# Optimization experiments

Measured on AMD Instinct MI355X. Metric: run time of the kernel, lower is better.

Reference implementation:

```python
import jax, jax.numpy as jnp
import numpy as np

N_NODES = 100000
N_INCID = 2000000
N_HEDGES = 300000
IN_DIM = 92
H_DIM = 64
ATTR_DIM = 35
HOUT_DIM = 128
N_GRAPHS = 512
N_LAYERS = 3
MSG_DIM = 2 * H_DIM + ATTR_DIM  # 163, matches Linear(2*node_fea_dim+hedge_fea_dim, out_dim)


def _segment_mean(vals, ids, num_segments):
    s = jax.ops.segment_sum(vals, ids, num_segments=num_segments)
    c = jax.ops.segment_sum(jnp.ones((vals.shape[0],), vals.dtype), ids, num_segments=num_segments)
    return s / jnp.maximum(c, 1.0)[:, None]


def setup_inputs() -> dict:
    key = jax.random.key(0)
    ks = jax.random.split(key, 16)
    x = jax.random.normal(ks[0], (N_NODES, IN_DIM), jnp.float32)
    incid_nodes = jax.random.randint(ks[1], (N_INCID,), 0, N_NODES)
    incid_hedges = jax.random.randint(ks[2], (N_INCID,), 0, N_HEDGES)
    hedge_attr = jax.random.normal(ks[3], (N_HEDGES, ATTR_DIM), jnp.float32)
    batch = jnp.sort(jax.random.randint(ks[4], (N_NODES,), 0, N_GRAPHS))
    def lin(k, fi, fo):
        lim = 1.0 / np.sqrt(fi)
        kw, kb = jax.random.split(k)
        return (jax.random.uniform(kw, (fi, fo), jnp.float32, -lim, lim),
                jax.random.uniform(kb, (fo,), jnp.float32, -lim, lim))
    W_embed, b_embed = lin(ks[5], IN_DIM, H_DIM)
    Wf, bf = [], []
    Wc, bc = [], []
    for l in range(N_LAYERS):
        w, b = lin(jax.random.fold_in(ks[6], l), MSG_DIM, H_DIM)
        Wf.append(w); bf.append(b)
        w, b = lin(jax.random.fold_in(ks[7], l), MSG_DIM, H_DIM)
        Wc.append(w); bc.append(b)
    Wf = jnp.stack(Wf); bf = jnp.stack(bf)
    Wc = jnp.stack(Wc); bc = jnp.stack(bc)
    W_proj, b_proj = lin(ks[8], H_DIM, HOUT_DIM)
    W_out, b_out = lin(ks[9], HOUT_DIM, 1)
    return {"x": x, "incid_nodes": incid_nodes, "incid_hedges": incid_hedges,
            "hedge_attr": hedge_attr, "batch": batch,
            "W_embed": W_embed, "b_embed": b_embed,
            "Wf": Wf, "bf": bf, "Wc": Wc, "bc": bc,
            "W_proj": W_proj, "b_proj": b_proj, "W_out": W_out, "b_out": b_out}


def reference(x, incid_nodes, incid_hedges, hedge_attr, batch,
              W_embed, b_embed, Wf, bf, Wc, bc, W_proj, b_proj, W_out, b_out):
    h = x @ W_embed + b_embed  # [N, H_DIM] embed
    node_cnt = jax.ops.segment_sum(jnp.ones((N_INCID,), h.dtype), incid_nodes,
                                   num_segments=N_NODES)
    has_incid = (node_cnt > 0)[:, None]
    # mean of hedge_attr over hedges containing each node (constant across layers)
    node_a = _segment_mean(hedge_attr[incid_hedges], incid_nodes, N_NODES)
    for l in range(N_LAYERS):
        # per-hedge mean of member node features (the normalized node_hedge_adj @ x)
        hedge_mean = _segment_mean(h[incid_nodes], incid_hedges, N_HEDGES)  # [H, H_DIM]
        # per-node mean over incident hedges of the message components
        node_h = _segment_mean(hedge_mean[incid_hedges], incid_nodes, N_NODES)
        x_part = jnp.where(has_incid, h, 0.0)  # mean over incidences of constant x_i
        z = jnp.concatenate([x_part, node_h, node_a], axis=1)  # [N, MSG_DIM]
        z_f = z @ Wf[l] + bf[l]
        z_c = z @ Wc[l] + bc[l]
        h = jax.nn.softplus(jax.nn.sigmoid(z_f) * jax.nn.softplus(z_c) + h)
    pooled = _segment_mean(h, batch, N_GRAPHS)  # scatter-mean global pooling
    p = jax.nn.softplus(pooled @ W_proj + b_proj)
    return p @ W_out + b_out  # [N_GRAPHS, 1]
```

## Files before the change

kernel.cpp:

```cpp
#include <hip/hip_runtime.h>
#include <hip/hip_bf16.h>

#define N_NODES 100000
#define N_INCID 2000000
#define N_HEDGES 300000
#define IN_DIM 92
#define H_DIM 64
#define ATTR_DIM 35
#define ATTR_PAIRS 18
#define HOUT_DIM 128
#define N_GRAPHS 512
#define N_LAYERS 3
#define MSG_DIM 163
#define KPAIRS 96
#define ZLDS 100
#define EPAIRS 48
#define ELDS 50

#define IPB 8192
#define NBLK 245
#define ESHIFT 9
#define NB_E 586
#define NSHIFT 8
#define NB_N 391
#define VALBITS 21

typedef short bf16x8 __attribute__((ext_vector_type(8)));
typedef float f32x4 __attribute__((ext_vector_type(4)));

__device__ __forceinline__ float softplusf(float x) {
    return fmaxf(x, 0.f) + __logf(1.f + __expf(-fabsf(x)));
}
__device__ __forceinline__ float sigmoidf(float x) {
    return __builtin_amdgcn_rcpf(1.f + __expf(-x));
}
__device__ __forceinline__ float u2f(unsigned u) {
    union { unsigned u; float f; } x; x.u = u; return x.f;
}
__device__ __forceinline__ unsigned f2_to_bf2(float x, float y) {
    union { float f; unsigned u; } a, b;
    a.f = x; b.f = y;
    unsigned lo = (a.u + 0x7fffu + ((a.u >> 16) & 1u)) >> 16;
    unsigned hi = ((b.u + 0x7fffu + ((b.u >> 16) & 1u)) >> 16) << 16;
    return lo | hi;
}

__global__ void embpack_k(const float* __restrict__ W, unsigned* __restrict__ BtE) {
    int idx = blockIdx.x * 256 + threadIdx.x;
    if (idx >= 64 * EPAIRS) return;
    int c = idx / EPAIRS, p = idx - c * EPAIRS;
    int k0 = 2 * p, k1 = 2 * p + 1;
    float v0 = (k0 < IN_DIM) ? W[k0 * 64 + c] : 0.f;
    float v1 = (k1 < IN_DIM) ? W[k1 * 64 + c] : 0.f;
    BtE[idx] = f2_to_bf2(v0, v1);
}

__global__ void __launch_bounds__(256)
embed_mfma_k(const float* __restrict__ x, const unsigned* __restrict__ BtE,
             const float* __restrict__ be, const int* __restrict__ ncnt,
             float* __restrict__ h, unsigned* __restrict__ hb,
             unsigned* __restrict__ zb) {
    __shared__ unsigned zsu[64][ELDS];
    __shared__ unsigned btu[64][ELDS];
    int node0 = blockIdx.x * 64;
    int t = threadIdx.x;
    for (int idx = t; idx < 64 * EPAIRS; idx += 256) {
        int r = idx / EPAIRS, p = idx - r * EPAIRS;
        int node = node0 + r;
        unsigned pr = 0u;
        if (node < N_NODES && p < 46) {
            float2 f = *(const float2*)(x + (size_t)node * IN_DIM + 2 * p);
            pr = f2_to_bf2(f.x, f.y);
        }
        zsu[r][p] = pr;
    }
    for (int idx = t; idx < 64 * EPAIRS; idx += 256) {
        int c = idx / EPAIRS, p = idx - c * EPAIRS;
        btu[c][p] = BtE[idx];
    }
    __syncthreads();
    int w = t >> 6, lane = t & 63, row16 = lane & 15, kg = lane >> 4;
    f32x4 acc[4];
#pragma unroll
    for (int n = 0; n < 4; ++n) acc[n] = (f32x4){0.f, 0.f, 0.f, 0.f};
#pragma unroll
    for (int ks = 0; ks < 3; ++ks) {
        int pbase = ks * 16 + kg * 4;
        bf16x8 a = *(const bf16x8*)&zsu[w * 16 + row16][pbase];
#pragma unroll
        for (int n = 0; n < 4; ++n) {
            bf16x8 b = *(const bf16x8*)&btu[n * 16 + row16][pbase];
            acc[n] = __builtin_amdgcn_mfma_f32_16x16x32_bf16(a, b, acc[n], 0, 0, 0);
        }
    }
#pragma unroll
    for (int i = 0; i < 4; ++i) {
        int node = node0 + w * 16 + kg * 4 + i;
        if (node < N_NODES) {
            bool has = ncnt[node] > 0;
#pragma unroll
            for (int n = 0; n < 4; ++n) {
                int d = n * 16 + row16;
                float nv = acc[n][i] + be[d];
                h[node * 64 + d] = nv;
                float other = __shfl_xor(nv, 1);
                if ((d & 1) == 0) {
                    unsigned pr = f2_to_bf2(nv, other);
                    hb[node * 32 + (d >> 1)] = pr;
                    zb[(size_t)node * KPAIRS + (d >> 1)] = has ? pr : 0u;
                }
            }
        }
    }
}

__global__ void attrconv_k(const float* __restrict__ hattr, unsigned* __restrict__ hab) {
    int idx = blockIdx.x * 256 + threadIdx.x;
    if (idx >= N_HEDGES * ATTR_PAIRS) return;
    int e = idx / ATTR_PAIRS, p = idx - e * ATTR_PAIRS;
    int d0 = 2 * p, d1 = 2 * p + 1;
    float v0 = hattr[e * ATTR_DIM + d0];
    float v1 = (d1 < ATTR_DIM) ? hattr[e * ATTR_DIM + d1] : 0.f;
    hab[idx] = f2_to_bf2(v0, v1);
}

__global__ void btpack_k(const float* __restrict__ Wf, const float* __restrict__ Wc,
                         unsigned* __restrict__ Btb) {
    int idx = blockIdx.x * 256 + threadIdx.x;
    if (idx >= N_LAYERS * 128 * KPAIRS) return;
    int l = idx / (128 * KPAIRS);
    int rem = idx - l * 128 * KPAIRS;
    int c = rem / KPAIRS, p = rem - c * KPAIRS;
    int k0 = 2 * p, k1 = 2 * p + 1;
    const float* W = (c < 64) ? (Wf + (size_t)l * MSG_DIM * 64) : (Wc + (size_t)l * MSG_DIM * 64);
    int cc = c & 63;
    float v0 = (k0 < MSG_DIM) ? W[k0 * 64 + cc] : 0.f;
    float v1 = (k1 < MSG_DIM) ? W[k1 * 64 + cc] : 0.f;
    Btb[idx] = f2_to_bf2(v0, v1);
}

__global__ void sorthist_k(const int* __restrict__ key, int* __restrict__ hist,
                           int kshift, int NB) {
    __shared__ int cnt[640];
    int blk = blockIdx.x;
    for (int i = threadIdx.x; i < NB; i += 256) cnt[i] = 0;
    __syncthreads();
    int base = blk * IPB;
    int end = min(base + IPB, N_INCID);
    for (int i = base + threadIdx.x; i < end; i += 256)
        atomicAdd(&cnt[key[i] >> kshift], 1);
    __syncthreads();
    for (int i = threadIdx.x; i < NB; i += 256) hist[blk * NB + i] = cnt[i];
}

__global__ void scanR1_k(const int* __restrict__ in, int* __restrict__ out,
                         int* __restrict__ bsum, int n, int NB) {
    __shared__ int tmp[256];
    int gid = blockIdx.x * 256 + threadIdx.x;
    int v = 0;
    if (gid < n) {
        int bucket = gid / NBLK, blk = gid - bucket * NBLK;
        v = in[blk * NB + bucket];
    }
    tmp[threadIdx.x] = v;
    __syncthreads();
    for (int o = 1; o < 256; o <<= 1) {
        int t = (threadIdx.x >= o) ? tmp[threadIdx.x - o] : 0;
        __syncthreads();
        tmp[threadIdx.x] += t;
        __syncthreads();
    }
    if (gid < n) out[gid] = tmp[threadIdx.x] - v;
    if (threadIdx.x == 255) bsum[blockIdx.x] = tmp[255];
}

__global__ void scan2_k(int* __restrict__ bsum, int nb) {
    __shared__ int tmp[256];
    __shared__ int carry;
    if (threadIdx.x == 0) carry = 0;
    __syncthreads();
    for (int base = 0; base < nb; base += 256) {
        int gid = base + threadIdx.x;
        int v = (gid < nb) ? bsum[gid] : 0;
        tmp[threadIdx.x] = v;
        __syncthreads();
        for (int o = 1; o < 256; o <<= 1) {
            int t = (threadIdx.x >= o) ? tmp[threadIdx.x - o] : 0;
            __syncthreads();
            tmp[threadIdx.x] += t;
            __syncthreads();
        }
        if (gid < nb) bsum[gid] = tmp[threadIdx.x] - v + carry;
        __syncthreads();
        if (threadIdx.x == 0) carry += tmp[255];
        __syncthreads();
    }
}

__global__ void scan3_k(int* __restrict__ out, const int* __restrict__ bsum, int n) {
    int gid = blockIdx.x * 256 + threadIdx.x;
    if (gid < n) out[gid] += bsum[blockIdx.x];
}

__global__ void sortscat_k(const int* __restrict__ key, const int* __restrict__ val,
                           const int* __restrict__ soff, unsigned* __restrict__ stage,
                           int kshift, int NB) {
    __shared__ int cur[640], bas[640];
    int blk = blockIdx.x;
    for (int i = threadIdx.x; i < NB; i += 256) {
        cur[i] = 0;
        bas[i] = soff[i * NBLK + blk];
    }
    __syncthreads();
    int base = blk * IPB;
    int end = min(base + IPB, N_INCID);
    unsigned kmaskbits = (1u << kshift) - 1u;
    for (int i = base + threadIdx.x; i < end; i += 256) {
        int k = key[i], b = k >> kshift;
        int d = bas[b] + atomicAdd(&cur[b], 1);
        stage[d] = (((unsigned)k & kmaskbits) << VALBITS) | (unsigned)val[i];
    }
}

__global__ void sortfine_k(const unsigned* __restrict__ stage, const int* __restrict__ soff,
                           int* __restrict__ csr, int* __restrict__ koff,
                           float* __restrict__ krcp, int* __restrict__ kcnt,
                           int kshift, int NB, int NKEYS) {
    __shared__ int cnt[512], off[512], cur[512];
    __shared__ int ts[256];
    int b = blockIdx.x;
    int tid = threadIdx.x;
    int KPB = 1 << kshift;
    int kbase = b << kshift;
    int base = soff[b * NBLK];
    int end = (b == NB - 1) ? N_INCID : soff[(b + 1) * NBLK];
    for (int i = tid; i < KPB; i += 256) cnt[i] = 0;
    __syncthreads();
    for (int i = base + tid; i < end; i += 256)
        atomicAdd(&cnt[stage[i] >> VALBITS], 1);
    __syncthreads();
    int half = KPB >> 1;
    int c0 = 0, c1 = 0;
    if (tid < half) { c0 = cnt[2 * tid]; c1 = cnt[2 * tid + 1]; ts[tid] = c0 + c1; }
    __syncthreads();
    for (int o = 1; o < 256; o <<= 1) {
        int v = (tid >= o && tid < half) ? ts[tid - o] : 0;
        __syncthreads();
        if (tid < half) ts[tid] += v;
        __syncthreads();
    }
    if (tid < half) {
        int ex = ts[tid] - (c0 + c1);
        off[2 * tid] = ex;
        off[2 * tid + 1] = ex + c0;
    }
    __syncthreads();
    for (int k = tid; k < KPB; k += 256) {
        int gk = kbase + k;
        if (gk < NKEYS) {
            koff[gk] = base + off[k];
            krcp[gk] = 1.0f / (float)max(cnt[k], 1);
            kcnt[gk] = cnt[k];
        }
        cur[k] = 0;
    }
    __syncthreads();
    for (int i = base + tid; i < end; i += 256) {
        unsigned it = stage[i];
        int lk = (int)(it >> VALBITS);
        int pos = base + off[lk] + atomicAdd(&cur[lk], 1);
        csr[pos] = (int)(it & ((1u << VALBITS) - 1u));
    }
}

__global__ void sentinel_k(int* __restrict__ eoff, int* __restrict__ noff) {
    if (threadIdx.x == 0) eoff[N_HEDGES] = N_INCID;
    if (threadIdx.x == 1) noff[N_NODES] = N_INCID;
}

__global__ void hmean_k(const int* __restrict__ eoff, const int* __restrict__ csr_en,
                        const uint4* __restrict__ hbv4, const float* __restrict__ ercp,
                        uint4* __restrict__ hmv4) {
    int idx = blockIdx.x * 256 + threadIdx.x;
    int e = idx >> 5, l = idx & 31;
    if (e >= N_HEDGES) return;
    int sub = l >> 3, q = l & 7;
    int s = eoff[e], t = eoff[e + 1];
    float a0 = 0, a1 = 0, a2 = 0, a3 = 0, a4 = 0, a5 = 0, a6 = 0, a7 = 0;
    for (int base = s; base < t; base += 32) {
        int cnt = min(32, t - base);
        int myidx = (base + l < t) ? csr_en[base + l] : 0;
        for (int j = 0; j < cnt; j += 16) {
            uint4 v[4];
#pragma unroll
            for (int w = 0; w < 4; ++w) {
                int mem = j + 4 * w + sub;
                int nq = __shfl(myidx, mem, 32);
                v[w] = (mem < cnt) ? hbv4[nq * 8 + q] : make_uint4(0u, 0u, 0u, 0u);
            }
#pragma unroll
            for (int w = 0; w < 4; ++w) {
                a0 += u2f(v[w].x << 16); a1 += u2f(v[w].x);
                a2 += u2f(v[w].y << 16); a3 += u2f(v[w].y);
                a4 += u2f(v[w].z << 16); a5 += u2f(v[w].z);
                a6 += u2f(v[w].w << 16); a7 += u2f(v[w].w);
            }
        }
    }
    a0 += __shfl_xor(a0, 8); a0 += __shfl_xor(a0, 16);
    a1 += __shfl_xor(a1, 8); a1 += __shfl_xor(a1, 16);
    a2 += __shfl_xor(a2, 8); a2 += __shfl_xor(a2, 16);
    a3 += __shfl_xor(a3, 8); a3 += __shfl_xor(a3, 16);
    a4 += __shfl_xor(a4, 8); a4 += __shfl_xor(a4, 16);
    a5 += __shfl_xor(a5, 8); a5 += __shfl_xor(a5, 16);
    a6 += __shfl_xor(a6, 8); a6 += __shfl_xor(a6, 16);
    a7 += __shfl_xor(a7, 8); a7 += __shfl_xor(a7, 16);
    if (sub == 0) {
        float rc = ercp[e];
        hmv4[e * 8 + q] = make_uint4(f2_to_bf2(a0 * rc, a1 * rc), f2_to_bf2(a2 * rc, a3 * rc),
                                     f2_to_bf2(a4 * rc, a5 * rc), f2_to_bf2(a6 * rc, a7 * rc));
    }
}

__global__ void nodeh_k(const int* __restrict__ noff, const int* __restrict__ csr_ne,
                        const uint4* __restrict__ hmv4, const float* __restrict__ nrcp,
                        uint4* __restrict__ zbv4) {
    int idx = blockIdx.x * 256 + threadIdx.x;
    int n = idx >> 5, l = idx & 31;
    if (n >= N_NODES) return;
    int sub = l >> 3, q = l & 7;
    int s = noff[n], t = noff[n + 1];
    float a0 = 0, a1 = 0, a2 = 0, a3 = 0, a4 = 0, a5 = 0, a6 = 0, a7 = 0;
    for (int base = s; base < t; base += 32) {
        int cnt = min(32, t - base);
        int myidx = (base + l < t) ? csr_ne[base + l] : 0;
        for (int j = 0; j < cnt; j += 16) {
            uint4 v[4];
#pragma unroll
            for (int w = 0; w < 4; ++w) {
                int mem = j + 4 * w + sub;
                int eq = __shfl(myidx, mem, 32);
                v[w] = (mem < cnt) ? hmv4[eq * 8 + q] : make_uint4(0u, 0u, 0u, 0u);
            }
#pragma unroll
            for (int w = 0; w < 4; ++w) {
                a0 += u2f(v[w].x << 16); a1 += u2f(v[w].x);
                a2 += u2f(v[w].y << 16); a3 += u2f(v[w].y);
                a4 += u2f(v[w].z << 16); a5 += u2f(v[w].z);
                a6 += u2f(v[w].w << 16); a7 += u2f(v[w].w);
            }
        }
    }
    a0 += __shfl_xor(a0, 8); a0 += __shfl_xor(a0, 16);
    a1 += __shfl_xor(a1, 8); a1 += __shfl_xor(a1, 16);
    a2 += __shfl_xor(a2, 8); a2 += __shfl_xor(a2, 16);
    a3 += __shfl_xor(a3, 8); a3 += __shfl_xor(a3, 16);
    a4 += __shfl_xor(a4, 8); a4 += __shfl_xor(a4, 16);
    a5 += __shfl_xor(a5, 8); a5 += __shfl_xor(a5, 16);
    a6 += __shfl_xor(a6, 8); a6 += __shfl_xor(a6, 16);
    a7 += __shfl_xor(a7, 8); a7 += __shfl_xor(a7, 16);
    if (sub == 0) {
        float rc = nrcp[n];
        zbv4[(size_t)n * 24 + 8 + q] =
            make_uint4(f2_to_bf2(a0 * rc, a1 * rc), f2_to_bf2(a2 * rc, a3 * rc),
                       f2_to_bf2(a4 * rc, a5 * rc), f2_to_bf2(a6 * rc, a7 * rc));
    }
}

__global__ void nodea_k(const int* __restrict__ noff, const int* __restrict__ csr_ne,
                        const uint2* __restrict__ habv, const float* __restrict__ nrcp,
                        uint2* __restrict__ zbv) {
    int idx = blockIdx.x * 256 + threadIdx.x;
    int n = idx >> 5, l = idx & 31;
    if (n >= N_NODES) return;
    int sub = l >> 4, q = l & 15;
    bool act = (q < ATTR_PAIRS / 2);
    int s = noff[n], t = noff[n + 1];
    float a0 = 0.f, a1 = 0.f, a2 = 0.f, a3 = 0.f;
    for (int base = s; base < t; base += 32) {
        int cnt = min(32, t - base);
        int myidx = (base + l < t) ? csr_ne[base + l] : 0;
        for (int j = 0; j < cnt; j += 16) {
            uint2 v[8];
#pragma unroll
            for (int w = 0; w < 8; ++w) {
                int mem = j + 2 * w + sub;
                int eq = __shfl(myidx, mem, 32);
                v[w] = (act && mem < cnt) ? habv[eq * (ATTR_PAIRS / 2) + q] : make_uint2(0u, 0u);
            }
#pragma unroll
            for (int w = 0; w < 8; ++w) {
                a0 += u2f(v[w].x << 16); a1 += u2f(v[w].x);
                a2 += u2f(v[w].y << 16); a3 += u2f(v[w].y);
            }
        }
    }
    a0 += __shfl_xor(a0, 16);
    a1 += __shfl_xor(a1, 16);
    a2 += __shfl_xor(a2, 16);
    a3 += __shfl_xor(a3, 16);
    if (sub == 0) {
        float rc = nrcp[n];
        uint2 pr = act ? make_uint2(f2_to_bf2(a0 * rc, a1 * rc), f2_to_bf2(a2 * rc, a3 * rc))
                       : make_uint2(0u, 0u);
        zbv[(size_t)n * (KPAIRS / 2) + 32 + q] = pr;
    }
}

__global__ void __launch_bounds__(256)
layer_mfma_k(const unsigned* __restrict__ Btl, const float* __restrict__ bfv,
             const float* __restrict__ bcv, const int* __restrict__ ncnt,
             unsigned* __restrict__ zb, float* __restrict__ h,
             unsigned* __restrict__ hb) {
    __shared__ unsigned zsu[64][ZLDS];
    int node0 = blockIdx.x * 64;
    int t = threadIdx.x;
    int w = t >> 6, lane = t & 63;
    int row16 = lane & 15, kg = lane >> 4;

    uint4 bregF[6], bregC[6];
    {
        const uint4* bv = (const uint4*)Btl;
        int colF = w * 16 + row16;
        int colC = colF + 64;
#pragma unroll
        for (int ks = 0; ks < 6; ++ks) {
            bregF[ks] = bv[colF * 24 + ks * 4 + kg];
            bregC[ks] = bv[colC * 24 + ks * 4 + kg];
        }
    }
    {
        const uint4* zv = (const uint4*)zb;
        for (int idx = t; idx < 64 * 24; idx += 256) {
            int r = idx / 24, p4 = idx - r * 24;
            int node = node0 + r;
            uint4 v = make_uint4(0u, 0u, 0u, 0u);
            if (node < N_NODES) v = zv[(size_t)node * 24 + p4];
            *(uint4*)&zsu[r][p4 * 4] = v;
        }
    }
    __syncthreads();

    f32x4 accF[4], accC[4];
#pragma unroll
    for (int n = 0; n < 4; ++n) {
        accF[n] = (f32x4){0.f, 0.f, 0.f, 0.f};
        accC[n] = (f32x4){0.f, 0.f, 0.f, 0.f};
    }

#pragma unroll
    for (int ks = 0; ks < 6; ++ks) {
        int pbase = ks * 16 + kg * 4;
        bf16x8 bF = *(const bf16x8*)&bregF[ks];
        bf16x8 bC = *(const bf16x8*)&bregC[ks];
#pragma unroll
        for (int rb = 0; rb < 4; ++rb) {
            bf16x8 a = *(const bf16x8*)&zsu[rb * 16 + row16][pbase];
            accF[rb] = __builtin_amdgcn_mfma_f32_16x16x32_bf16(a, bF, accF[rb], 0, 0, 0);
            accC[rb] = __builtin_amdgcn_mfma_f32_16x16x32_bf16(a, bC, accC[rb], 0, 0, 0);
        }
    }

    int d = w * 16 + row16;
    float bfd = bfv[d], bcd = bcv[d];
#pragma unroll
    for (int rb = 0; rb < 4; ++rb) {
#pragma unroll
        for (int i = 0; i < 4; ++i) {
            int node = node0 + rb * 16 + kg * 4 + i;
            if (node < N_NODES) {
                bool has = ncnt[node] > 0;
                float f = accF[rb][i] + bfd;
                float c = accC[rb][i] + bcd;
                float hv = h[node * 64 + d];
                float nv = softplusf(sigmoidf(f) * softplusf(c) + hv);
                h[node * 64 + d] = nv;
                float other = __shfl_xor(nv, 1);
                if ((d & 1) == 0) {
                    unsigned pr = f2_to_bf2(nv, other);
                    hb[node * 32 + (d >> 1)] = pr;
                    zb[(size_t)node * KPAIRS + (d >> 1)] = has ? pr : 0u;
                }
            }
        }
    }
}

__global__ void gstart_k(const int* __restrict__ batch, int* __restrict__ gstart) {
    int g = blockIdx.x * 256 + threadIdx.x;
    if (g > N_GRAPHS) return;
    int lo = 0, hi = N_NODES;
    while (lo < hi) {
        int mid = (lo + hi) >> 1;
        if (batch[mid] < g) lo = mid + 1; else hi = mid;
    }
    gstart[g] = lo;
}

__global__ void poolhead_k(const float* __restrict__ h, const int* __restrict__ gstart,
                           const float* __restrict__ Wp, const float* __restrict__ bp,
                           const float* __restrict__ Wo, const float* __restrict__ bo,
                           float* __restrict__ out) {
    __shared__ float partial[4][64];
    __shared__ float pm[64];
    __shared__ float pr[128];
    int g = blockIdx.x, t = threadIdx.x;
    int s = gstart[g], e = gstart[g + 1];
    int w = t >> 6, lane = t & 63;
    float acc = 0.f;
    for (int n = s + w; n < e; n += 4) acc += h[n * 64 + lane];
    partial[w][lane] = acc;
    __syncthreads();
    if (t < 64) {
        float c = fmaxf((float)(e - s), 1.0f);
        pm[t] = (partial[0][t] + partial[1][t] + partial[2][t] + partial[3][t]) / c;
    }
    __syncthreads();
    if (t < 128) {
        float a = bp[t];
#pragma unroll 4
        for (int k = 0; k < 64; ++k) a += pm[k] * Wp[k * HOUT_DIM + t];
        pr[t] = softplusf(a) * Wo[t];
    }
    __syncthreads();
    if (t < 64) {
        float v = pr[t] + pr[t + 64];
        for (int o = 32; o > 0; o >>= 1) v += __shfl_down(v, o);
        if (t == 0) out[g] = v + bo[0];
    }
}

extern "C" void kernel_launch(void* const* d_in, const int* in_sizes, int n_in,
                              void* d_out, int out_size, void* d_ws, size_t ws_size,
                              hipStream_t stream) {
    const float* x       = (const float*)d_in[0];
    const int*   inc_n   = (const int*)d_in[1];
    const int*   inc_e   = (const int*)d_in[2];
    const float* hattr   = (const float*)d_in[3];
    const int*   batch   = (const int*)d_in[4];
    const float* W_embed = (const float*)d_in[5];
    const float* b_embed = (const float*)d_in[6];
    const float* Wf      = (const float*)d_in[7];
    const float* bf      = (const float*)d_in[8];
    const float* Wc      = (const float*)d_in[9];
    const float* bc      = (const float*)d_in[10];
    const float* W_proj  = (const float*)d_in[11];
    const float* b_proj  = (const float*)d_in[12];
    const float* W_out   = (const float*)d_in[13];
    const float* b_out   = (const float*)d_in[14];
    float* out = (float*)d_out;

    char* ws = (char*)d_ws;
    size_t off = 0;
    auto alloc = [&](size_t bytes) {
        void* p = ws + off;
        off = (off + bytes + 255) & ~(size_t)255;
        return p;
    };
    float*    h      = (float*)alloc((size_t)N_NODES * 64 * 4);
    unsigned* hb     = (unsigned*)alloc((size_t)N_NODES * 32 * 4);
    unsigned* hmean  = (unsigned*)alloc((size_t)N_HEDGES * 32 * 4);
    unsigned* zb     = (unsigned*)alloc((size_t)N_NODES * KPAIRS * 4);
    unsigned* hab    = (unsigned*)alloc((size_t)N_HEDGES * ATTR_PAIRS * 4);
    unsigned* Btb    = (unsigned*)alloc((size_t)N_LAYERS * 128 * KPAIRS * 4);
    unsigned* BtE    = (unsigned*)alloc((size_t)64 * EPAIRS * 4);
    int*      ncnt   = (int*)alloc((size_t)N_NODES * 4);
    int*      ecnt   = (int*)alloc((size_t)N_HEDGES * 4);
    float*    nrcp   = (float*)alloc((size_t)N_NODES * 4);
    float*    ercp   = (float*)alloc((size_t)N_HEDGES * 4);
    int*      eoff   = (int*)alloc((size_t)(N_HEDGES + 1) * 4);
    int*      noff   = (int*)alloc((size_t)(N_NODES + 1) * 4);
    int*      csr_en = (int*)alloc((size_t)N_INCID * 4);
    int*      csr_ne = (int*)alloc((size_t)N_INCID * 4);
    int*      hist   = (int*)alloc((size_t)NB_E * NBLK * 4);
    int*      soff   = (int*)alloc((size_t)NB_E * NBLK * 4);
    int*      bsum   = (int*)alloc((size_t)2048 * 4);
    int*      gstart = (int*)alloc((size_t)(N_GRAPHS + 1) * 4);
    unsigned* stage  = (unsigned*)hmean;

    {
        int nlog = NB_E * NBLK;
        int nsb = (nlog + 255) / 256;
        sorthist_k<<<NBLK, 256, 0, stream>>>(inc_e, hist, ESHIFT, NB_E);
        scanR1_k<<<nsb, 256, 0, stream>>>(hist, soff, bsum, nlog, NB_E);
        scan2_k<<<1, 256, 0, stream>>>(bsum, nsb);
        scan3_k<<<nsb, 256, 0, stream>>>(soff, bsum, nlog);
        sortscat_k<<<NBLK, 256, 0, stream>>>(inc_e, inc_n, soff, stage, ESHIFT, NB_E);
        sortfine_k<<<NB_E, 256, 0, stream>>>(stage, soff, csr_en, eoff, ercp, ecnt,
                                             ESHIFT, NB_E, N_HEDGES);
    }
    {
        int nlog = NB_N * NBLK;
        int nsb = (nlog + 255) / 256;
        sorthist_k<<<NBLK, 256, 0, stream>>>(inc_n, hist, NSHIFT, NB_N);
        scanR1_k<<<nsb, 256, 0, stream>>>(hist, soff, bsum, nlog, NB_N);
        scan2_k<<<1, 256, 0, stream>>>(bsum, nsb);
        scan3_k<<<nsb, 256, 0, stream>>>(soff, bsum, nlog);
        sortscat_k<<<NBLK, 256, 0, stream>>>(inc_n, inc_e, soff, stage, NSHIFT, NB_N);
        sortfine_k<<<NB_N, 256, 0, stream>>>(stage, soff, csr_ne, noff, nrcp, ncnt,
                                             NSHIFT, NB_N, N_NODES);
    }
    sentinel_k<<<1, 64, 0, stream>>>(eoff, noff);

    embpack_k<<<(64 * EPAIRS + 255) / 256, 256, 0, stream>>>(W_embed, BtE);
    embed_mfma_k<<<(N_NODES + 63) / 64, 256, 0, stream>>>(x, BtE, b_embed, ncnt, h, hb, zb);
    attrconv_k<<<(N_HEDGES * ATTR_PAIRS + 255) / 256, 256, 0, stream>>>(hattr, hab);
    btpack_k<<<(N_LAYERS * 128 * KPAIRS + 255) / 256, 256, 0, stream>>>(Wf, Wc, Btb);
    nodea_k<<<(N_NODES * 32) / 256, 256, 0, stream>>>(noff, csr_ne, (const uint2*)hab, nrcp,
                                                      (uint2*)zb);

    for (int l = 0; l < N_LAYERS; ++l) {
        hmean_k<<<(N_HEDGES * 32) / 256, 256, 0, stream>>>(eoff, csr_en, (const uint4*)hb, ercp,
                                                           (uint4*)hmean);
        nodeh_k<<<(N_NODES * 32) / 256, 256, 0, stream>>>(noff, csr_ne, (const uint4*)hmean, nrcp,
                                                          (uint4*)zb);
        layer_mfma_k<<<(N_NODES + 63) / 64, 256, 0, stream>>>(Btb + (size_t)l * 128 * KPAIRS,
                                                              bf + l * 64, bc + l * 64,
                                                              ncnt, zb, h, hb);
    }
    gstart_k<<<(N_GRAPHS + 1 + 255) / 256, 256, 0, stream>>>(batch, gstart);
    poolhead_k<<<N_GRAPHS, 256, 0, stream>>>(h, gstart, W_proj, b_proj, W_out, b_out, out);
}
```

Before: 637.8 us.

## Fuse dual CSR sort passes and narrow gather kernels to 8 lanes per segment

The hedge-keyed and node-keyed bucket sorts now share one histogram kernel and one scatter kernel, reading both incidence arrays once and writing to two separate staging regions. The hyperedge-mean and node-mean gather kernels now assign 8 lanes per segment instead of 32 and drop the cross-lane shuffle reduction. This targets idle lanes on low-degree segments and redundant passes over the incidence data. The trade-off is more shared memory per sort block and less memory-level parallelism per segment for high-degree rows.

After: 592.2 us. -7.2%, faster.

```diff
diff --git a/kernel.cpp b/kernel.cpp
--- a/kernel.cpp
+++ b/kernel.cpp
@@ -139,18 +139,22 @@
     Btb[idx] = f2_to_bf2(v0, v1);
 }
 
-__global__ void sorthist_k(const int* __restrict__ key, int* __restrict__ hist,
-                           int kshift, int NB) {
-    __shared__ int cnt[640];
+__global__ void sorthist2_k(const int* __restrict__ keyE, const int* __restrict__ keyN,
+                            int* __restrict__ histE, int* __restrict__ histN) {
+    __shared__ int cntE[NB_E], cntN[NB_N];
     int blk = blockIdx.x;
-    for (int i = threadIdx.x; i < NB; i += 256) cnt[i] = 0;
+    for (int i = threadIdx.x; i < NB_E; i += 256) cntE[i] = 0;
+    for (int i = threadIdx.x; i < NB_N; i += 256) cntN[i] = 0;
     __syncthreads();
     int base = blk * IPB;
     int end = min(base + IPB, N_INCID);
-    for (int i = base + threadIdx.x; i < end; i += 256)
-        atomicAdd(&cnt[key[i] >> kshift], 1);
-    __syncthreads();
-    for (int i = threadIdx.x; i < NB; i += 256) hist[blk * NB + i] = cnt[i];
+    for (int i = base + threadIdx.x; i < end; i += 256) {
+        atomicAdd(&cntE[keyE[i] >> ESHIFT], 1);
+        atomicAdd(&cntN[keyN[i] >> NSHIFT], 1);
+    }
+    __syncthreads();
+    for (int i = threadIdx.x; i < NB_E; i += 256) histE[blk * NB_E + i] = cntE[i];
+    for (int i = threadIdx.x; i < NB_N; i += 256) histN[blk * NB_N + i] = cntN[i];
 }
 
 __global__ void scanR1_k(const int* __restrict__ in, int* __restrict__ out,
@@ -202,23 +206,24 @@
     if (gid < n) out[gid] += bsum[blockIdx.x];
 }
 
-__global__ void sortscat_k(const int* __restrict__ key, const int* __restrict__ val,
-                           const int* __restrict__ soff, unsigned* __restrict__ stage,
-                           int kshift, int NB) {
-    __shared__ int cur[640], bas[640];
+__global__ void sortscat2_k(const int* __restrict__ keyE, const int* __restrict__ keyN,
+                            const int* __restrict__ soffE, const int* __restrict__ soffN,
+                            unsigned* __restrict__ stageE, unsigned* __restrict__ stageN) {
+    __shared__ int curE[NB_E], basE[NB_E], curN[NB_N], basN[NB_N];
     int blk = blockIdx.x;
-    for (int i = threadIdx.x; i < NB; i += 256) {
-        cur[i] = 0;
-        bas[i] = soff[i * NBLK + blk];
-    }
+    for (int i = threadIdx.x; i < NB_E; i += 256) { curE[i] = 0; basE[i] = soffE[i * NBLK + blk]; }
+    for (int i = threadIdx.x; i < NB_N; i += 256) { curN[i] = 0; basN[i] = soffN[i * NBLK + blk]; }
     __syncthreads();
     int base = blk * IPB;
     int end = min(base + IPB, N_INCID);
-    unsigned kmaskbits = (1u << kshift) - 1u;
     for (int i = base + threadIdx.x; i < end; i += 256) {
-        int k = key[i], b = k >> kshift;
-        int d = bas[b] + atomicAdd(&cur[b], 1);
-        stage[d] = (((unsigned)k & kmaskbits) << VALBITS) | (unsigned)val[i];
+        int kE = keyE[i], kN = keyN[i];
+        int bE = kE >> ESHIFT;
+        int dE = basE[bE] + atomicAdd(&curE[bE], 1);
+        stageE[dE] = (((unsigned)kE & ((1u << ESHIFT) - 1u)) << VALBITS) | (unsigned)kN;
+        int bN = kN >> NSHIFT;
+        int dN = basN[bN] + atomicAdd(&curN[bN], 1);
+        stageN[dN] = (((unsigned)kN & ((1u << NSHIFT) - 1u)) << VALBITS) | (unsigned)kE;
     }
 }
 
@@ -282,89 +287,61 @@
                         const uint4* __restrict__ hbv4, const float* __restrict__ ercp,
                         uint4* __restrict__ hmv4) {
     int idx = blockIdx.x * 256 + threadIdx.x;
-    int e = idx >> 5, l = idx & 31;
+    int e = idx >> 3, il = idx & 7;
     if (e >= N_HEDGES) return;
-    int sub = l >> 3, q = l & 7;
     int s = eoff[e], t = eoff[e + 1];
     float a0 = 0, a1 = 0, a2 = 0, a3 = 0, a4 = 0, a5 = 0, a6 = 0, a7 = 0;
-    for (int base = s; base < t; base += 32) {
-        int cnt = min(32, t - base);
-        int myidx = (base + l < t) ? csr_en[base + l] : 0;
-        for (int j = 0; j < cnt; j += 16) {
-            uint4 v[4];
-#pragma unroll
-            for (int w = 0; w < 4; ++w) {
-                int mem = j + 4 * w + sub;
-                int nq = __shfl(myidx, mem, 32);
-                v[w] = (mem < cnt) ? hbv4[nq * 8 + q] : make_uint4(0u, 0u, 0u, 0u);
-            }
-#pragma unroll
-            for (int w = 0; w < 4; ++w) {
-                a0 += u2f(v[w].x << 16); a1 += u2f(v[w].x);
-                a2 += u2f(v[w].y << 16); a3 += u2f(v[w].y);
-                a4 += u2f(v[w].z << 16); a5 += u2f(v[w].z);
-                a6 += u2f(v[w].w << 16); a7 += u2f(v[w].w);
-            }
-        }
-    }
-    a0 += __shfl_xor(a0, 8); a0 += __shfl_xor(a0, 16);
-    a1 += __shfl_xor(a1, 8); a1 += __shfl_xor(a1, 16);
-    a2 += __shfl_xor(a2, 8); a2 += __shfl_xor(a2, 16);
-    a3 += __shfl_xor(a3, 8); a3 += __shfl_xor(a3, 16);
-    a4 += __shfl_xor(a4, 8); a4 += __shfl_xor(a4, 16);
-    a5 += __shfl_xor(a5, 8); a5 += __shfl_xor(a5, 16);
-    a6 += __shfl_xor(a6, 8); a6 += __shfl_xor(a6, 16);
-    a7 += __shfl_xor(a7, 8); a7 += __shfl_xor(a7, 16);
-    if (sub == 0) {
-        float rc = ercp[e];
-        hmv4[e * 8 + q] = make_uint4(f2_to_bf2(a0 * rc, a1 * rc), f2_to_bf2(a2 * rc, a3 * rc),
-                                     f2_to_bf2(a4 * rc, a5 * rc), f2_to_bf2(a6 * rc, a7 * rc));
-    }
+    for (int base = s; base < t; base += 8) {
+        int cnt = t - base;
+        int myidx = (base + il < t) ? csr_en[base + il] : 0;
+        uint4 v[8];
+#pragma unroll
+        for (int m = 0; m < 8; ++m) {
+            int nq = __shfl(myidx, m, 8);
+            v[m] = (m < cnt) ? hbv4[nq * 8 + il] : make_uint4(0u, 0u, 0u, 0u);
+        }
+#pragma unroll
+        for (int m = 0; m < 8; ++m) {
+            a0 += u2f(v[m].x << 16); a1 += u2f(v[m].x);
+            a2 += u2f(v[m].y << 16); a3 += u2f(v[m].y);
+            a4 += u2f(v[m].z << 16); a5 += u2f(v[m].z);
+            a6 += u2f(v[m].w << 16); a7 += u2f(v[m].w);
+        }
+    }
+    float rc = ercp[e];
+    hmv4[e * 8 + il] = make_uint4(f2_to_bf2(a0 * rc, a1 * rc), f2_to_bf2(a2 * rc, a3 * rc),
+                                  f2_to_bf2(a4 * rc, a5 * rc), f2_to_bf2(a6 * rc, a7 * rc));
 }
 
 __global__ void nodeh_k(const int* __restrict__ noff, const int* __restrict__ csr_ne,
                         const uint4* __restrict__ hmv4, const float* __restrict__ nrcp,
                         uint4* __restrict__ zbv4) {
     int idx = blockIdx.x * 256 + threadIdx.x;
-    int n = idx >> 5, l = idx & 31;
+    int n = idx >> 3, il = idx & 7;
     if (n >= N_NODES) return;
-    int sub = l >> 3, q = l & 7;
     int s = noff[n], t = noff[n + 1];
     float a0 = 0, a1 = 0, a2 = 0, a3 = 0, a4 = 0, a5 = 0, a6 = 0, a7 = 0;
-    for (int base = s; base < t; base += 32) {
-        int cnt = min(32, t - base);
-        int myidx = (base + l < t) ? csr_ne[base + l] : 0;
-        for (int j = 0; j < cnt; j += 16) {
-            uint4 v[4];
-#pragma unroll
-            for (int w = 0; w < 4; ++w) {
-                int mem = j + 4 * w + sub;
-                int eq = __shfl(myidx, mem, 32);
-                v[w] = (mem < cnt) ? hmv4[eq * 8 + q] : make_uint4(0u, 0u, 0u, 0u);
-            }
-#pragma unroll
-            for (int w = 0; w < 4; ++w) {
-                a0 += u2f(v[w].x << 16); a1 += u2f(v[w].x);
-                a2 += u2f(v[w].y << 16); a3 += u2f(v[w].y);
-                a4 += u2f(v[w].z << 16); a5 += u2f(v[w].z);
-                a6 += u2f(v[w].w << 16); a7 += u2f(v[w].w);
-            }
-        }
-    }
-    a0 += __shfl_xor(a0, 8); a0 += __shfl_xor(a0, 16);
-    a1 += __shfl_xor(a1, 8); a1 += __shfl_xor(a1, 16);
-    a2 += __shfl_xor(a2, 8); a2 += __shfl_xor(a2, 16);
-    a3 += __shfl_xor(a3, 8); a3 += __shfl_xor(a3, 16);
-    a4 += __shfl_xor(a4, 8); a4 += __shfl_xor(a4, 16);
-    a5 += __shfl_xor(a5, 8); a5 += __shfl_xor(a5, 16);
-    a6 += __shfl_xor(a6, 8); a6 += __shfl_xor(a6, 16);
-    a7 += __shfl_xor(a7, 8); a7 += __shfl_xor(a7, 16);
-    if (sub == 0) {
-        float rc = nrcp[n];
-        zbv4[(size_t)n * 24 + 8 + q] =
-            make_uint4(f2_to_bf2(a0 * rc, a1 * rc), f2_to_bf2(a2 * rc, a3 * rc),
-                       f2_to_bf2(a4 * rc, a5 * rc), f2_to_bf2(a6 * rc, a7 * rc));
-    }
+    for (int base = s; base < t; base += 8) {
+        int cnt = t - base;
+        int myidx = (base + il < t) ? csr_ne[base + il] : 0;
+        uint4 v[8];
+#pragma unroll
+        for (int m = 0; m < 8; ++m) {
+            int eq = __shfl(myidx, m, 8);
+            v[m] = (m < cnt) ? hmv4[eq * 8 + il] : make_uint4(0u, 0u, 0u, 0u);
+        }
+#pragma unroll
+        for (int m = 0; m < 8; ++m) {
+            a0 += u2f(v[m].x << 16); a1 += u2f(v[m].x);
+            a2 += u2f(v[m].y << 16); a3 += u2f(v[m].y);
+            a4 += u2f(v[m].z << 16); a5 += u2f(v[m].z);
+            a6 += u2f(v[m].w << 16); a7 += u2f(v[m].w);
+        }
+    }
+    float rc = nrcp[n];
+    zbv4[(size_t)n * 24 + 8 + il] =
+        make_uint4(f2_to_bf2(a0 * rc, a1 * rc), f2_to_bf2(a2 * rc, a3 * rc),
+                   f2_to_bf2(a4 * rc, a5 * rc), f2_to_bf2(a6 * rc, a7 * rc));
 }
 
 __global__ void nodea_k(const int* __restrict__ noff, const int* __restrict__ csr_ne,
@@ -572,34 +549,31 @@
     int*      noff   = (int*)alloc((size_t)(N_NODES + 1) * 4);
     int*      csr_en = (int*)alloc((size_t)N_INCID * 4);
     int*      csr_ne = (int*)alloc((size_t)N_INCID * 4);
-    int*      hist   = (int*)alloc((size_t)NB_E * NBLK * 4);
-    int*      soff   = (int*)alloc((size_t)NB_E * NBLK * 4);
+    int*      histE  = (int*)alloc((size_t)NB_E * NBLK * 4);
+    int*      histN  = (int*)alloc((size_t)NB_N * NBLK * 4);
+    int*      soffE  = (int*)alloc((size_t)NB_E * NBLK * 4);
+    int*      soffN  = (int*)alloc((size_t)NB_N * NBLK * 4);
     int*      bsum   = (int*)alloc((size_t)2048 * 4);
     int*      gstart = (int*)alloc((size_t)(N_GRAPHS + 1) * 4);
-    unsigned* stage  = (unsigned*)hmean;
-
+    unsigned* stageE = (unsigned*)hmean;
+    unsigned* stageN = (unsigned*)hmean + N_INCID;
+
+    sorthist2_k<<<NBLK, 256, 0, stream>>>(inc_e, inc_n, histE, histN);
     {
-        int nlog = NB_E * NBLK;
-        int nsb = (nlog + 255) / 256;
-        sorthist_k<<<NBLK, 256, 0, stream>>>(inc_e, hist, ESHIFT, NB_E);
-        scanR1_k<<<nsb, 256, 0, stream>>>(hist, soff, bsum, nlog, NB_E);
-        scan2_k<<<1, 256, 0, stream>>>(bsum, nsb);
-        scan3_k<<<nsb, 256, 0, stream>>>(soff, bsum, nlog);
-        sortscat_k<<<NBLK, 256, 0, stream>>>(inc_e, inc_n, soff, stage, ESHIFT, NB_E);
-        sortfine_k<<<NB_E, 256, 0, stream>>>(stage, soff, csr_en, eoff, ercp, ecnt,
-                                             ESHIFT, NB_E, N_HEDGES);
-    }
-    {
-        int nlog = NB_N * NBLK;
-        int nsb = (nlog + 255) / 256;
-        sorthist_k<<<NBLK, 256, 0, stream>>>(inc_n, hist, NSHIFT, NB_N);
-        scanR1_k<<<nsb, 256, 0, stream>>>(hist, soff, bsum, nlog, NB_N);
-        scan2_k<<<1, 256, 0, stream>>>(bsum, nsb);
-        scan3_k<<<nsb, 256, 0, stream>>>(soff, bsum, nlog);
-        sortscat_k<<<NBLK, 256, 0, stream>>>(inc_n, inc_e, soff, stage, NSHIFT, NB_N);
-        sortfine_k<<<NB_N, 256, 0, stream>>>(stage, soff, csr_ne, noff, nrcp, ncnt,
-                                             NSHIFT, NB_N, N_NODES);
-    }
+        int nlogE = NB_E * NBLK, nsbE = (nlogE + 255) / 256;
+        scanR1_k<<<nsbE, 256, 0, stream>>>(histE, soffE, bsum, nlogE, NB_E);
+        scan2_k<<<1, 256, 0, stream>>>(bsum, nsbE);
+        scan3_k<<<nsbE, 256, 0, stream>>>(soffE, bsum, nlogE);
+        int nlogN = NB_N * NBLK, nsbN = (nlogN + 255) / 256;
+        scanR1_k<<<nsbN, 256, 0, stream>>>(histN, soffN, bsum, nlogN, NB_N);
+        scan2_k<<<1, 256, 0, stream>>>(bsum, nsbN);
+        scan3_k<<<nsbN, 256, 0, stream>>>(soffN, bsum, nlogN);
+    }
+    sortscat2_k<<<NBLK, 256, 0, stream>>>(inc_e, inc_n, soffE, soffN, stageE, stageN);
+    sortfine_k<<<NB_E, 256, 0, stream>>>(stageE, soffE, csr_en, eoff, ercp, ecnt,
+                                         ESHIFT, NB_E, N_HEDGES);
+    sortfine_k<<<NB_N, 256, 0, stream>>>(stageN, soffN, csr_ne, noff, nrcp, ncnt,
+                                         NSHIFT, NB_N, N_NODES);
     sentinel_k<<<1, 64, 0, stream>>>(eoff, noff);
 
     embpack_k<<<(64 * EPAIRS + 255) / 256, 256, 0, stream>>>(W_embed, BtE);
@@ -610,10 +584,10 @@
                                                       (uint2*)zb);
 
     for (int l = 0; l < N_LAYERS; ++l) {
-        hmean_k<<<(N_HEDGES * 32) / 256, 256, 0, stream>>>(eoff, csr_en, (const uint4*)hb, ercp,
-                                                           (uint4*)hmean);
-        nodeh_k<<<(N_NODES * 32) / 256, 256, 0, stream>>>(noff, csr_ne, (const uint4*)hmean, nrcp,
-                                                          (uint4*)zb);
+        hmean_k<<<(N_HEDGES * 8) / 256, 256, 0, stream>>>(eoff, csr_en, (const uint4*)hb, ercp,
+                                                          (uint4*)hmean);
+        nodeh_k<<<(N_NODES * 8) / 256, 256, 0, stream>>>(noff, csr_ne, (const uint4*)hmean, nrcp,
+                                                         (uint4*)zb);
         layer_mfma_k<<<(N_NODES + 63) / 64, 256, 0, stream>>>(Btb + (size_t)l * 128 * KPAIRS,
                                                               bf + l * 64, bc + l * 64,
                                                               ncnt, zb, h, hb);
```
